# Optimization experiments

Measured on AMD Instinct MI355X. Metric: run time of the kernel, lower is better.

Reference implementation:

```python
import jax, jax.numpy as jnp
import numpy as np

LPB = 0.03   # lower_probability_bound
LEB = 0.2    # lower_entropy_bound
UEB = 0.5    # upper_entropy_bound
BETA = 1.0
N, K, S, D = 8192, 1000, 8, 1024


def setup_inputs() -> dict:
    key = jax.random.key(0)
    k1, k2, k3 = jax.random.split(key, 3)
    x = jax.random.normal(k1, (N, D), dtype=jnp.float32)
    # per-sample logit temperature so entropies spread across the gating band
    base = jax.random.normal(k2, (N, K), dtype=jnp.float32)
    scales = jax.random.uniform(k3, (N, 1), dtype=jnp.float32, minval=1.0, maxval=15.0)
    text_logits = base * scales
    memory = jnp.zeros((K, S, D), dtype=jnp.float32)
    # init_entropy(prop_max=1): -log(1/K) = log(K)
    memory_entropy = jnp.full((K, S), jnp.log(jnp.float32(K)), dtype=jnp.float32)
    memory_state = jnp.zeros((K, S), dtype=bool)
    return {"x": x, "text_logits": text_logits, "memory": memory,
            "memory_entropy": memory_entropy, "memory_state": memory_state}


def _update_memory(memory, memory_entropy, memory_state, x, text_logits):
    """Sequential entropy-gated scatter update (order-dependent, as in torch loop)."""
    def step(carry, inp):
        mem, ent, st = carry
        xi, li = inp                      # xi: [D], li: [K]
        p = jax.nn.softmax(li)
        lab = jnp.argmax(li)
        H = -jnp.sum(jnp.log(p + 1e-6) * p)  # shannon entropy
        row = ent[lab]                    # [S] entropies of this class's slots
        cond = (p[lab] > LPB) & (H > LEB) & (H < UEB) & jnp.any(H < row)
        idx = jnp.argmax(row)             # evict highest-entropy slot
        mem = mem.at[lab, idx].set(jnp.where(cond, xi, mem[lab, idx]))
        ent = ent.at[lab, idx].set(jnp.where(cond, H, ent[lab, idx]))
        st = st.at[lab, idx].set(jnp.where(cond, True, st[lab, idx]))
        return (mem, ent, st), cond

    (mem, ent, st), selected = jax.lax.scan(
        step, (memory, memory_entropy, memory_state), (x, text_logits))
    return mem, ent, st, selected


def reference(x, text_logits, memory, memory_entropy, memory_state):
    mem, ent, st, selected = _update_memory(memory, memory_entropy, memory_state, x, text_logits)
    # get_logits: A_ = (memory @ x.T).permute(2,0,1) -> [N, K, S]
    A_ = jnp.einsum('ksd,nd->nks', mem, x)
    logits = -jnp.sum(jnp.exp(-BETA * (1.0 - A_)), axis=-1)  # [N, K]
    return logits
```

## Files before the change

### kernel.cpp

```cpp
#include <hip/hip_runtime.h>
#include <hip/hip_bf16.h>
#include <math.h>

#define NN 8192
#define KK 1000
#define SS 8
#define DD 1024
#define RR (KK * SS)
#define RRP 8192

typedef __bf16 bf16x8 __attribute__((ext_vector_type(8)));
typedef float f32x4 __attribute__((ext_vector_type(4)));
typedef unsigned short ushort_t;
typedef ushort_t ushort8 __attribute__((ext_vector_type(8)));

static __device__ __forceinline__ ushort_t f2bf(float f) {
  unsigned u = __float_as_uint(f);
  unsigned r = (u + 0x7FFFu + ((u >> 16) & 1u)) >> 16;
  return (ushort_t)r;
}

#define GLD16(gsrc, ldst)                                                     \
  __builtin_amdgcn_global_load_lds(                                           \
      (const __attribute__((address_space(1))) unsigned int*)(gsrc),          \
      (__attribute__((address_space(3))) unsigned int*)(ldst), 16, 0, 0)

#define SBAR() asm volatile("s_barrier" ::: "memory")
#define WAITVM(n) asm volatile("s_waitcnt vmcnt(" #n ")" ::: "memory")

__global__ __launch_bounds__(256) void stats_kernel(
    const float* __restrict__ tl, int2* __restrict__ cand) {
  const int wid = (blockIdx.x * 256 + threadIdx.x) >> 6;
  const int l = threadIdx.x & 63;
  if (wid >= NN) return;
  const float* row = tl + (size_t)wid * KK;

  float vf[16];
  bool vld[4];
  #pragma unroll
  for (int c = 0; c < 4; ++c) {
    const int base = c * 256 + l * 4;
    vld[c] = (base <= KK - 4);
    if (vld[c]) {
      const float4 v = *(const float4*)(row + base);
      vf[c * 4 + 0] = v.x; vf[c * 4 + 1] = v.y;
      vf[c * 4 + 2] = v.z; vf[c * 4 + 3] = v.w;
    } else {
      vf[c * 4 + 0] = vf[c * 4 + 1] = vf[c * 4 + 2] = vf[c * 4 + 3] = -INFINITY;
    }
  }

  float m = -INFINITY; int bi = 1 << 30;
  #pragma unroll
  for (int c = 0; c < 4; ++c)
    #pragma unroll
    for (int j = 0; j < 4; ++j) {
      const float val = vf[c * 4 + j];
      if (val > m) { m = val; bi = c * 256 + l * 4 + j; }
    }
  #pragma unroll
  for (int off = 32; off > 0; off >>= 1) {
    const float om = __shfl_xor(m, off);
    const int ob = __shfl_xor(bi, off);
    if (om > m || (om == m && ob < bi)) { m = om; bi = ob; }
  }

  float z = 0.f;
  #pragma unroll
  for (int c = 0; c < 4; ++c)
    if (vld[c])
      #pragma unroll
      for (int j = 0; j < 4; ++j) z += expf(vf[c * 4 + j] - m);
  #pragma unroll
  for (int off = 32; off > 0; off >>= 1) z += __shfl_xor(z, off);

  float h = 0.f;
  #pragma unroll
  for (int c = 0; c < 4; ++c)
    if (vld[c])
      #pragma unroll
      for (int j = 0; j < 4; ++j) {
        const float p = expf(vf[c * 4 + j] - m) / z;
        h -= p * logf(p + 1e-6f);
      }
  #pragma unroll
  for (int off = 32; off > 0; off >>= 1) h += __shfl_xor(h, off);

  if (l == 0) {
    const float plab = 1.0f / z;
    const bool c = (plab > 0.03f) && (h > 0.2f) && (h < 0.5f);
    cand[wid] = make_int2(c ? bi : -1, __float_as_int(h));
  }
}

__global__ __launch_bounds__(256) void select_kernel(
    const int2* __restrict__ cand, const float* __restrict__ ment,
    int* __restrict__ sel) {
  const int w = threadIdx.x >> 6;
  const int l = threadIdx.x & 63;
  const int k = blockIdx.x * 4 + w;
  if (k >= KK) return;

  float ent[SS]; int idx[SS];
  #pragma unroll
  for (int s = 0; s < SS; ++s) { ent[s] = ment[k * SS + s]; idx[s] = -1; }

  for (int base = 0; base < NN; base += 64) {
    const int2 c = cand[base + l];
    unsigned long long msk = __ballot(c.x == k);
    while (msk) {
      const int src = __ffsll((long long)msk) - 1;
      msk &= msk - 1;
      const float H = __shfl(__int_as_float(c.y), src);
      float mx = ent[0]; int mi = 0;
      #pragma unroll
      for (int s = 1; s < SS; ++s) if (ent[s] > mx) { mx = ent[s]; mi = s; }
      if (H < mx) { ent[mi] = H; idx[mi] = base + src; }
    }
  }
  if (l == 0) {
    #pragma unroll
    for (int s = 0; s < SS; ++s) sel[k * SS + s] = idx[s];
  }
}

__global__ __launch_bounds__(128) void convgather_kernel(
    const float* __restrict__ x, const float* __restrict__ mem,
    const int* __restrict__ sel, ushort_t* __restrict__ xb,
    ushort_t* __restrict__ Bb) {
  const int r = blockIdx.x;
  const int t = threadIdx.x;
  const float* src;
  ushort_t* dst;
  if (r < NN) {
    src = x + (size_t)r * DD;
    dst = xb + (size_t)r * DD;
  } else {
    const int rr = r - NN;
    dst = Bb + (size_t)rr * DD;
    if (rr >= RR) {
      *(ushort8*)(dst + t * 8) = (ushort8)0;
      return;
    }
    const int sl = sel[rr];
    src = (sl >= 0) ? (x + (size_t)sl * DD) : (mem + (size_t)rr * DD);
  }
  const float4 a = *(const float4*)(src + t * 8);
  const float4 b = *(const float4*)(src + t * 8 + 4);
  ushort8 o;
  o[0] = f2bf(a.x); o[1] = f2bf(a.y); o[2] = f2bf(a.z); o[3] = f2bf(a.w);
  o[4] = f2bf(b.x); o[5] = f2bf(b.y); o[6] = f2bf(b.z); o[7] = f2bf(b.w);
  *(ushort8*)(dst + t * 8) = o;
}

#define BKS 64
#define NTS (DD / BKS)
#define LDSH 32768

__global__ __launch_bounds__(512, 2) void logits_kernel(
    const ushort_t* __restrict__ xb, const ushort_t* __restrict__ Bb,
    float* __restrict__ out) {
  __shared__ ushort_t lds[2 * LDSH];
  const int t = threadIdx.x;
  const int w = t >> 6;
  const int l = t & 63;
  const int wm = w >> 2;
  const int wn = w & 3;
  const int n0 = blockIdx.x * 256;
  const int r0 = blockIdx.y * 256;

  const int srow = w * 8 + (l >> 3);
  const int gcolh = (((l & 7) ^ ((l >> 3) & 7)) << 3);
  const ushort_t* gA = xb + (size_t)(n0 + srow) * DD + gcolh;
  const ushort_t* gB = Bb + (size_t)(r0 + srow) * DD + gcolh;

#define STAGE_AC(T, c)                                                        \
  GLD16(gA + (size_t)(c) * 64 * DD + (size_t)(T) * BKS,                       \
        lds + ((T) & 1) * LDSH + (c) * 4096 + w * 512)
#define STAGE_BC(T, c)                                                        \
  GLD16(gB + (size_t)(c) * 64 * DD + (size_t)(T) * BKS,                       \
        lds + ((T) & 1) * LDSH + 16384 + (c) * 4096 + w * 512)

  const int lr = l & 15;
  const int ch = l >> 4;
  const int kc0 = ((ch ^ (lr & 7)) << 3);
  const int kc1 = (((4 + ch) ^ (lr & 7)) << 3);
  const int arow = (wm * 128 + lr) * 64;
  const int brow = 16384 + (wn * 64 + lr) * 64;

  f32x4 acc[8][4];
  #pragma unroll
  for (int mi = 0; mi < 8; ++mi)
    #pragma unroll
    for (int ni = 0; ni < 4; ++ni) acc[mi][ni] = (f32x4){0.f, 0.f, 0.f, 0.f};

  STAGE_AC(0, 0); STAGE_AC(0, 2);
  STAGE_BC(0, 0); STAGE_BC(0, 2);
  STAGE_BC(0, 1); STAGE_BC(0, 3);
  STAGE_AC(0, 1); STAGE_AC(0, 3);
  WAITVM(2);
  SBAR();

#define MFMA_CLUSTER(q)                                                       \
  do {                                                                        \
    __builtin_amdgcn_sched_barrier(0);                                        \
    __builtin_amdgcn_s_setprio(1);                                            \
    _Pragma("unroll")                                                         \
    for (int i = 0; i < 2; ++i)                                               \
      _Pragma("unroll")                                                       \
      for (int ni = 0; ni < 4; ++ni)                                          \
        acc[2 * (q) + i][ni] = __builtin_amdgcn_mfma_f32_16x16x32_bf16(       \
            af[i][0], bf[ni][0], acc[2 * (q) + i][ni], 0, 0, 0);              \
    _Pragma("unroll")                                                         \
    for (int i = 0; i < 2; ++i)                                               \
      _Pragma("unroll")                                                       \
      for (int ni = 0; ni < 4; ++ni)                                          \
        acc[2 * (q) + i][ni] = __builtin_amdgcn_mfma_f32_16x16x32_bf16(       \
            af[i][1], bf[ni][1], acc[2 * (q) + i][ni], 0, 0, 0);              \
    __builtin_amdgcn_s_setprio(0);                                            \
    __builtin_amdgcn_sched_barrier(0);                                        \
  } while (0)

  #pragma unroll 2
  for (int T = 0; T < NTS; ++T) {
    const ushort_t* buf = lds + (T & 1) * LDSH;
    const int Tn = T + 1;
    const bool st = (Tn < NTS);
    bf16x8 bf[4][2];
    bf16x8 af[2][2];

    #pragma unroll
    for (int ni = 0; ni < 4; ++ni) {
      bf[ni][0] = *(const bf16x8*)(buf + brow + ni * 1024 + kc0);
      bf[ni][1] = *(const bf16x8*)(buf + brow + ni * 1024 + kc1);
    }
    af[0][0] = *(const bf16x8*)(buf + arow + kc0);
    af[0][1] = *(const bf16x8*)(buf + arow + kc1);
    af[1][0] = *(const bf16x8*)(buf + arow + 1024 + kc0);
    af[1][1] = *(const bf16x8*)(buf + arow + 1024 + kc1);
    if (st) { STAGE_AC(Tn, 0); STAGE_AC(Tn, 2); }
    SBAR();
    MFMA_CLUSTER(0);
    SBAR();

    af[0][0] = *(const bf16x8*)(buf + arow + 2048 + kc0);
    af[0][1] = *(const bf16x8*)(buf + arow + 2048 + kc1);
    af[1][0] = *(const bf16x8*)(buf + arow + 3072 + kc0);
    af[1][1] = *(const bf16x8*)(buf + arow + 3072 + kc1);
    if (st) { STAGE_BC(Tn, 0); STAGE_BC(Tn, 2); }
    SBAR();
    MFMA_CLUSTER(1);
    SBAR();

    if (T < NTS - 1) { WAITVM(4); } else { WAITVM(0); }
    af[0][0] = *(const bf16x8*)(buf + arow + 4096 + kc0);
    af[0][1] = *(const bf16x8*)(buf + arow + 4096 + kc1);
    af[1][0] = *(const bf16x8*)(buf + arow + 5120 + kc0);
    af[1][1] = *(const bf16x8*)(buf + arow + 5120 + kc1);
    if (st) { STAGE_BC(Tn, 1); STAGE_BC(Tn, 3); }
    SBAR();
    MFMA_CLUSTER(2);
    SBAR();

    af[0][0] = *(const bf16x8*)(buf + arow + 6144 + kc0);
    af[0][1] = *(const bf16x8*)(buf + arow + 6144 + kc1);
    af[1][0] = *(const bf16x8*)(buf + arow + 7168 + kc0);
    af[1][1] = *(const bf16x8*)(buf + arow + 7168 + kc1);
    if (st) { STAGE_AC(Tn, 1); STAGE_AC(Tn, 3); }
    SBAR();
    MFMA_CLUSTER(3);
    WAITVM(2);
    SBAR();
  }

  const int rbase = n0 + wm * 128 + ((l >> 4) * 4);
  #pragma unroll
  for (int mi = 0; mi < 8; ++mi) {
    #pragma unroll
    for (int ni = 0; ni < 4; ++ni) {
      const int colbase = r0 + wn * 64 + ni * 16 + (l & 15);
      const int cls = colbase >> 3;
      #pragma unroll
      for (int rg = 0; rg < 4; ++rg) {
        float e = __expf(acc[mi][ni][rg] - 1.0f);
        e += __shfl_xor(e, 1);
        e += __shfl_xor(e, 2);
        e += __shfl_xor(e, 4);
        if ((l & 7) == 0 && cls < KK) {
          out[(size_t)(rbase + mi * 16 + rg) * KK + cls] = -fminf(e, 3.0e38f);
        }
      }
    }
  }
}

extern "C" void kernel_launch(void* const* d_in, const int* in_sizes, int n_in,
                              void* d_out, int out_size, void* d_ws, size_t ws_size,
                              hipStream_t stream) {
  const float* x    = (const float*)d_in[0];
  const float* tl   = (const float*)d_in[1];
  const float* mem  = (const float*)d_in[2];
  const float* ment = (const float*)d_in[3];
  float* out = (float*)d_out;

  char* ws = (char*)d_ws;
  int2*     cand = (int2*)ws;
  int*      sel  = (int*)(ws + NN * 8);
  ushort_t* Bb   = (ushort_t*)(ws + (1 << 20));
  ushort_t* xb   = (ushort_t*)(ws + (1 << 20) + (size_t)RRP * DD * 2);

  hipLaunchKernelGGL(stats_kernel, dim3(NN / 4), dim3(256), 0, stream, tl, cand);
  hipLaunchKernelGGL(select_kernel, dim3(250), dim3(256), 0, stream, cand, ment, sel);
  hipLaunchKernelGGL(convgather_kernel, dim3(NN + RRP), dim3(128), 0, stream,
                     x, mem, sel, xb, Bb);
  hipLaunchKernelGGL(logits_kernel, dim3(32, 32), dim3(512), 0, stream, xb, Bb, out);
}
```

Measured before the change: 224.1 us.

## Replace 256x256 GEMM tile with simpler 128x128 BK32 double-buffered kernel

Rewrites the logits GEMM kernel from a 256x256 tile, 512-thread, 4-phase interleaved pipeline into a 128x128 tile with 256 threads, K-step 32 and a plain double buffer. The grid shrinks its column dimension to 63 blocks, skipping the zero-padded rows beyond 8000. The goal is higher occupancy, smaller LDS use and less padded work. In exchange, each element is reused less, so global and LDS traffic per flop rises, and the simpler scheduling hides load latency less well.

```diff
diff --git a/kernel.cpp b/kernel.cpp
--- a/kernel.cpp
+++ b/kernel.cpp
@@ -153,132 +153,81 @@
   *(ushort8*)(dst + t * 8) = o;
 }
 
-#define BKS 64
-#define NTS (DD / BKS)
-#define LDSH 32768
-
-__global__ __launch_bounds__(512, 2) void logits_kernel(
+#define BK32 32
+#define NT32 (DD / BK32)
+
+__global__ __launch_bounds__(256) void logits_kernel(
     const ushort_t* __restrict__ xb, const ushort_t* __restrict__ Bb,
     float* __restrict__ out) {
-  __shared__ ushort_t lds[2 * LDSH];
+  __shared__ ushort_t lds[2 * 8192];
   const int t = threadIdx.x;
   const int w = t >> 6;
   const int l = t & 63;
-  const int wm = w >> 2;
-  const int wn = w & 3;
-  const int n0 = blockIdx.x * 256;
-  const int r0 = blockIdx.y * 256;
-
-  const int srow = w * 8 + (l >> 3);
-  const int gcolh = (((l & 7) ^ ((l >> 3) & 7)) << 3);
-  const ushort_t* gA = xb + (size_t)(n0 + srow) * DD + gcolh;
-  const ushort_t* gB = Bb + (size_t)(r0 + srow) * DD + gcolh;
-
-#define STAGE_AC(T, c)                                                        \
-  GLD16(gA + (size_t)(c) * 64 * DD + (size_t)(T) * BKS,                       \
-        lds + ((T) & 1) * LDSH + (c) * 4096 + w * 512)
-#define STAGE_BC(T, c)                                                        \
-  GLD16(gB + (size_t)(c) * 64 * DD + (size_t)(T) * BKS,                       \
-        lds + ((T) & 1) * LDSH + 16384 + (c) * 4096 + w * 512)
+  const int n0 = blockIdx.x * 128;
+  const int r0 = blockIdx.y * 128;
+  const int wr = (w >> 1) * 64;
+  const int wc = (w & 1) * 64;
+
+  const int srow = w * 16 + (l >> 2);
+  const int gcolh = (((l & 3) ^ ((l >> 3) & 3)) << 3);
+  const ushort_t* gA0 = xb + (size_t)(n0 + srow) * DD + gcolh;
+  const ushort_t* gA1 = xb + (size_t)(n0 + srow + 64) * DD + gcolh;
+  const ushort_t* gB0 = Bb + (size_t)(r0 + srow) * DD + gcolh;
+  const ushort_t* gB1 = Bb + (size_t)(r0 + srow + 64) * DD + gcolh;
+
+#define STAGE32(T) do {                                                       \
+    ushort_t* _b = lds + ((T) & 1) * 8192;                                    \
+    GLD16(gA0 + (size_t)(T) * BK32, _b + w * 512);                            \
+    GLD16(gA1 + (size_t)(T) * BK32, _b + 2048 + w * 512);                     \
+    GLD16(gB0 + (size_t)(T) * BK32, _b + 4096 + w * 512);                     \
+    GLD16(gB1 + (size_t)(T) * BK32, _b + 6144 + w * 512);                     \
+  } while (0)
 
   const int lr = l & 15;
-  const int ch = l >> 4;
-  const int kc0 = ((ch ^ (lr & 7)) << 3);
-  const int kc1 = (((4 + ch) ^ (lr & 7)) << 3);
-  const int arow = (wm * 128 + lr) * 64;
-  const int brow = 16384 + (wn * 64 + lr) * 64;
-
-  f32x4 acc[8][4];
-  #pragma unroll
-  for (int mi = 0; mi < 8; ++mi)
+  const int kb = ((l >> 4) * 16) ^ ((((lr) >> 1) & 3) << 4);
+
+  f32x4 acc[4][4];
+  #pragma unroll
+  for (int mi = 0; mi < 4; ++mi)
     #pragma unroll
     for (int ni = 0; ni < 4; ++ni) acc[mi][ni] = (f32x4){0.f, 0.f, 0.f, 0.f};
 
-  STAGE_AC(0, 0); STAGE_AC(0, 2);
-  STAGE_BC(0, 0); STAGE_BC(0, 2);
-  STAGE_BC(0, 1); STAGE_BC(0, 3);
-  STAGE_AC(0, 1); STAGE_AC(0, 3);
-  WAITVM(2);
+  STAGE32(0);
+  WAITVM(0);
   SBAR();
 
-#define MFMA_CLUSTER(q)                                                       \
-  do {                                                                        \
-    __builtin_amdgcn_sched_barrier(0);                                        \
-    __builtin_amdgcn_s_setprio(1);                                            \
-    _Pragma("unroll")                                                         \
-    for (int i = 0; i < 2; ++i)                                               \
-      _Pragma("unroll")                                                       \
-      for (int ni = 0; ni < 4; ++ni)                                          \
-        acc[2 * (q) + i][ni] = __builtin_amdgcn_mfma_f32_16x16x32_bf16(       \
-            af[i][0], bf[ni][0], acc[2 * (q) + i][ni], 0, 0, 0);              \
-    _Pragma("unroll")                                                         \
-    for (int i = 0; i < 2; ++i)                                               \
-      _Pragma("unroll")                                                       \
-      for (int ni = 0; ni < 4; ++ni)                                          \
-        acc[2 * (q) + i][ni] = __builtin_amdgcn_mfma_f32_16x16x32_bf16(       \
-            af[i][1], bf[ni][1], acc[2 * (q) + i][ni], 0, 0, 0);              \
-    __builtin_amdgcn_s_setprio(0);                                            \
-    __builtin_amdgcn_sched_barrier(0);                                        \
-  } while (0)
-
   #pragma unroll 2
-  for (int T = 0; T < NTS; ++T) {
-    const ushort_t* buf = lds + (T & 1) * LDSH;
-    const int Tn = T + 1;
-    const bool st = (Tn < NTS);
-    bf16x8 bf[4][2];
-    bf16x8 af[2][2];
-
+  for (int T = 0; T < NT32; ++T) {
+    const char* bufc = (const char*)(lds + (T & 1) * 8192);
+    if (T + 1 < NT32) STAGE32(T + 1);
+
+    bf16x8 af[4], bfr[4];
+    #pragma unroll
+    for (int mi = 0; mi < 4; ++mi)
+      af[mi] = *(const bf16x8*)(bufc + (wr + mi * 16 + lr) * 64 + kb);
+    #pragma unroll
+    for (int ni = 0; ni < 4; ++ni)
+      bfr[ni] = *(const bf16x8*)(bufc + 8192 + (wc + ni * 16 + lr) * 64 + kb);
+
+    __builtin_amdgcn_s_setprio(1);
+    #pragma unroll
+    for (int mi = 0; mi < 4; ++mi)
+      #pragma unroll
+      for (int ni = 0; ni < 4; ++ni)
+        acc[mi][ni] = __builtin_amdgcn_mfma_f32_16x16x32_bf16(
+            af[mi], bfr[ni], acc[mi][ni], 0, 0, 0);
+    __builtin_amdgcn_s_setprio(0);
+
+    WAITVM(0);
+    SBAR();
+  }
+
+  const int rbase = n0 + wr + ((l >> 4) * 4);
+  #pragma unroll
+  for (int mi = 0; mi < 4; ++mi) {
     #pragma unroll
     for (int ni = 0; ni < 4; ++ni) {
-      bf[ni][0] = *(const bf16x8*)(buf + brow + ni * 1024 + kc0);
-      bf[ni][1] = *(const bf16x8*)(buf + brow + ni * 1024 + kc1);
-    }
-    af[0][0] = *(const bf16x8*)(buf + arow + kc0);
-    af[0][1] = *(const bf16x8*)(buf + arow + kc1);
-    af[1][0] = *(const bf16x8*)(buf + arow + 1024 + kc0);
-    af[1][1] = *(const bf16x8*)(buf + arow + 1024 + kc1);
-    if (st) { STAGE_AC(Tn, 0); STAGE_AC(Tn, 2); }
-    SBAR();
-    MFMA_CLUSTER(0);
-    SBAR();
-
-    af[0][0] = *(const bf16x8*)(buf + arow + 2048 + kc0);
-    af[0][1] = *(const bf16x8*)(buf + arow + 2048 + kc1);
-    af[1][0] = *(const bf16x8*)(buf + arow + 3072 + kc0);
-    af[1][1] = *(const bf16x8*)(buf + arow + 3072 + kc1);
-    if (st) { STAGE_BC(Tn, 0); STAGE_BC(Tn, 2); }
-    SBAR();
-    MFMA_CLUSTER(1);
-    SBAR();
-
-    if (T < NTS - 1) { WAITVM(4); } else { WAITVM(0); }
-    af[0][0] = *(const bf16x8*)(buf + arow + 4096 + kc0);
-    af[0][1] = *(const bf16x8*)(buf + arow + 4096 + kc1);
-    af[1][0] = *(const bf16x8*)(buf + arow + 5120 + kc0);
-    af[1][1] = *(const bf16x8*)(buf + arow + 5120 + kc1);
-    if (st) { STAGE_BC(Tn, 1); STAGE_BC(Tn, 3); }
-    SBAR();
-    MFMA_CLUSTER(2);
-    SBAR();
-
-    af[0][0] = *(const bf16x8*)(buf + arow + 6144 + kc0);
-    af[0][1] = *(const bf16x8*)(buf + arow + 6144 + kc1);
-    af[1][0] = *(const bf16x8*)(buf + arow + 7168 + kc0);
-    af[1][1] = *(const bf16x8*)(buf + arow + 7168 + kc1);
-    if (st) { STAGE_AC(Tn, 1); STAGE_AC(Tn, 3); }
-    SBAR();
-    MFMA_CLUSTER(3);
-    WAITVM(2);
-    SBAR();
-  }
-
-  const int rbase = n0 + wm * 128 + ((l >> 4) * 4);
-  #pragma unroll
-  for (int mi = 0; mi < 8; ++mi) {
-    #pragma unroll
-    for (int ni = 0; ni < 4; ++ni) {
-      const int colbase = r0 + wn * 64 + ni * 16 + (l & 15);
+      const int colbase = r0 + wc + ni * 16 + (l & 15);
       const int cls = colbase >> 3;
       #pragma unroll
       for (int rg = 0; rg < 4; ++rg) {
@@ -313,5 +262,5 @@
   hipLaunchKernelGGL(select_kernel, dim3(250), dim3(256), 0, stream, cand, ment, sel);
   hipLaunchKernelGGL(convgather_kernel, dim3(NN + RRP), dim3(128), 0, stream,
                      x, mem, sel, xb, Bb);
-  hipLaunchKernelGGL(logits_kernel, dim3(32, 32), dim3(512), 0, stream, xb, Bb, out);
-}
+  hipLaunchKernelGGL(logits_kernel, dim3(64, 63), dim3(256), 0, stream, xb, Bb, out);
+}
```

New measurement: 240.8 us. +7.5%, slower.
